# Optimization experiments

Hardware: AMD Instinct MI355X
Metric: run time of the kernel (lower is better)

Reference implementation:

```python
import jax, jax.numpy as jnp
import numpy as np

K = 4                      # options['num_k']
NOISE_EPS = 0.1            # noise_epsilon in noisy_top_k_gating
LOSS_COEF = 1e-4
EPS_COMBINE = float(np.finfo(np.float64).eps)  # np.finfo(float).eps in combine
INV_SQRT2 = 0.7071067811865475


def _norm_cdf(z):
    # Normal(0,1).cdf
    return 0.5 * (1.0 + jax.lax.erf(z * INV_SQRT2))


def _cv_squared(v):
    # torch .var() is unbiased (ddof=1)
    return jnp.var(v, ddof=1) / (jnp.mean(v) ** 2 + 1e-10)


def setup_inputs() -> dict:
    key = jax.random.key(0)
    B, D, E, H, O = 1024, 1024, 16, 2048, 1024
    ks = jax.random.split(key, 6)
    x = jax.random.normal(ks[0], (B, D), jnp.float32)
    w_gate = jax.random.normal(ks[1], (D, E), jnp.float32) * 0.02
    w_noise = jax.random.normal(ks[2], (D, E), jnp.float32) * 0.02
    W1 = jax.random.normal(ks[3], (E, D, H), jnp.float32) / np.sqrt(D).astype(np.float32)
    b1 = jnp.zeros((E, H), jnp.float32)
    W2 = jax.random.normal(ks[4], (E, H, O), jnp.float32) / np.sqrt(H).astype(np.float32)
    b2 = jnp.zeros((E, O), jnp.float32)
    noise = jax.random.normal(ks[5], (B, E), jnp.float32)  # randn_like(clean_logits)
    return {"x": x, "w_gate": w_gate, "w_noise": w_noise,
            "W1": W1, "b1": b1, "W2": W2, "b2": b2, "noise": noise}


def moe_forward(x, w_gate, w_noise, W1, b1, W2, b2, noise):
    B = x.shape[0]
    # --- noisy top-k gating (train=True path) ---
    clean_logits = x @ w_gate                              # [B, E]
    noise_std = jax.nn.softplus(x @ w_noise) + NOISE_EPS   # [B, E]
    noisy_logits = clean_logits + noise * noise_std        # [B, E]
    top_logits, top_idx = jax.lax.top_k(noisy_logits, K + 1)  # [B, K+1]
    topk_gates = jax.nn.softmax(top_logits[:, :K], axis=1)    # [B, K]
    gates = jnp.zeros_like(noisy_logits).at[
        jnp.arange(B)[:, None], top_idx[:, :K]].set(topk_gates)  # [B, E] sparse
    # --- load = E[prob in top-k] (smooth load estimate) ---
    thr_in = top_logits[:, K][:, None]       # (k+1)-th value: threshold if in
    thr_out = top_logits[:, K - 1][:, None]  # k-th value: threshold if out
    is_in = noisy_logits > thr_in
    prob_if_in = _norm_cdf((clean_logits - thr_in) / noise_std)
    prob_if_out = _norm_cdf((clean_logits - thr_out) / noise_std)
    load = jnp.where(is_in, prob_if_in, prob_if_out).sum(0)   # [E]
    importance = gates.sum(0)                                 # [E]
    loss = (_cv_squared(importance) + _cv_squared(load)) * LOSS_COEF
    # --- experts + combine ---
    # Dense all-expert compute; gates are exactly zero off the top-k so the
    # gate-weighted sum reproduces the sparse dispatch/index_add combine math.
    h = jax.nn.relu(jnp.einsum('bi,eih->beh', x, W1) + b1)    # [B, E, H]
    expert_out = jnp.einsum('beh,eho->beo', h, W2) + b2       # [B, E, O]
    # combine: sum_e gate[b,e] * exp(expert_out[b,e,:]); zeros -> eps; log
    combined = jnp.einsum('be,beo->bo', gates, jnp.exp(expert_out))  # [B, O]
    combined = jnp.where(combined == 0, EPS_COMBINE, combined)
    y = jnp.log(combined)
    return y, loss


def reference(x, w_gate, w_noise, W1, b1, W2, b2, noise):
    return moe_forward(x, w_gate, w_noise, W1, b1, W2, b2, noise)
```

## Files before the change

### kernel.cpp

```cpp
#include <hip/hip_runtime.h>
#include <cstdint>
#include <cstddef>

#define BTOK 1024
#define DDIM 1024
#define EEXP 16
#define HDIM 2048
#define ODIM 1024

typedef __bf16 bh;
typedef bh bh8 __attribute__((ext_vector_type(8)));
typedef bh bh4 __attribute__((ext_vector_type(4)));
typedef float fx4 __attribute__((ext_vector_type(4)));

__device__ __forceinline__ void gload16(const void* g, void* l) {
  __builtin_amdgcn_global_load_lds(
      (const __attribute__((address_space(1))) void*)g,
      (__attribute__((address_space(3))) void*)l, 16, 0, 0);
}

__global__ __launch_bounds__(256) void k_tcvt(const float* __restrict__ in,
                                              bh* __restrict__ out, int R, int C) {
  const int e = blockIdx.z;
  const int r0 = blockIdx.y * 64, c0 = blockIdx.x * 64;
  const float* pin = in + (size_t)e * R * C;
  bh* pout = out + (size_t)e * R * C;
  __shared__ __align__(16) bh t[64 * 65];
  const int tid = threadIdx.x;
#pragma unroll
  for (int rep = 0; rep < 4; ++rep) {
    int task = rep * 256 + tid;
    int r = task >> 4, c4 = task & 15;
    fx4 v = *(const fx4*)(pin + (size_t)(r0 + r) * C + c0 + c4 * 4);
    int base = r * 65 + c4 * 4;
#pragma unroll
    for (int u = 0; u < 4; ++u) t[base + u] = (bh)v[u];
  }
  __syncthreads();
#pragma unroll
  for (int rep = 0; rep < 4; ++rep) {
    int task = rep * 256 + tid;
    int cc = task >> 4, g2 = task & 15;
    bh4 o;
#pragma unroll
    for (int u = 0; u < 4; ++u) o[u] = t[(g2 * 4 + u) * 65 + cc];
    *(bh4*)(pout + (size_t)(c0 + cc) * R + r0 + g2 * 4) = o;
  }
}

__global__ __launch_bounds__(256) void k_gating(
    const float* __restrict__ x, const float* __restrict__ wg,
    const float* __restrict__ wn, const float* __restrict__ nz,
    bh* __restrict__ xbf, unsigned* __restrict__ cnt,
    int* __restrict__ tok_buck, float* __restrict__ gate_buck,
    float* __restrict__ imp_part, float* __restrict__ load_part) {
  const int b = blockIdx.x, tid = threadIdx.x;
  __shared__ __align__(16) float xs[1024];
  __shared__ float part[32][9];
  __shared__ float vals[32];
  fx4 v = *(const fx4*)(x + (size_t)b * 1024 + tid * 4);
  *(fx4*)(xs + tid * 4) = v;
  bh4 xb;
#pragma unroll
  for (int u = 0; u < 4; ++u) xb[u] = (bh)v[u];
  *(bh4*)(xbf + (size_t)b * 1024 + tid * 4) = xb;
  __syncthreads();
  const int col = tid & 31, g = tid >> 5;
  const float* wp = ((col < 16) ? wg : wn) + (col & 15);
  float s = 0.f;
  for (int it = g * 128; it < g * 128 + 128; ++it) s += xs[it] * wp[it * 16];
  part[col][g] = s;
  __syncthreads();
  if (tid < 32) {
    float tsum = 0.f;
#pragma unroll
    for (int gg = 0; gg < 8; ++gg) tsum += part[tid][gg];
    vals[tid] = tsum;
  }
  __syncthreads();
  if (tid == 0) {
    float clean[16], sd[16], noisy[16];
#pragma unroll
    for (int e = 0; e < 16; ++e) {
      clean[e] = vals[e];
      float raw = vals[16 + e];
      float sp = fmaxf(raw, 0.f) + log1pf(expf(-fabsf(raw)));
      sd[e] = sp + 0.1f;
      noisy[e] = clean[e] + nz[b * 16 + e] * sd[e];
    }
    float tv[5]; int ti[5]; unsigned used = 0;
    for (int r = 0; r < 5; ++r) {
      float bst = -INFINITY; int bi = 0;
      for (int e = 0; e < 16; ++e)
        if (!((used >> e) & 1u) && noisy[e] > bst) { bst = noisy[e]; bi = e; }
      used |= 1u << bi; tv[r] = bst; ti[r] = bi;
    }
    float gts[4]; float se = 0.f;
#pragma unroll
    for (int k = 0; k < 4; ++k) { gts[k] = expf(tv[k] - tv[0]); se += gts[k]; }
#pragma unroll
    for (int k = 0; k < 4; ++k) gts[k] /= se;
    const float thr_in = tv[4], thr_out = tv[3];
    float imp[16];
#pragma unroll
    for (int e = 0; e < 16; ++e) imp[e] = 0.f;
    for (int k = 0; k < 4; ++k) imp[ti[k]] = gts[k];
    for (int e = 0; e < 16; ++e) imp_part[b * 16 + e] = imp[e];
    for (int e = 0; e < 16; ++e) {
      bool is_in = noisy[e] > thr_in;
      float z = (clean[e] - (is_in ? thr_in : thr_out)) / sd[e];
      load_part[b * 16 + e] = 0.5f * (1.f + erff(z * 0.70710678118654752f));
    }
    for (int k = 0; k < 4; ++k) {
      int ee = ti[k];
      unsigned p = atomicAdd(&cnt[ee], 1u);
      tok_buck[ee * 1024 + (int)p] = b;
      gate_buck[ee * 1024 + (int)p] = gts[k];
    }
  }
}

__device__ __forceinline__ float cv2_16(const float* v) {
  float m = 0.f;
  for (int i = 0; i < 16; ++i) m += v[i];
  m *= (1.f / 16.f);
  float var = 0.f;
  for (int i = 0; i < 16; ++i) { float d = v[i] - m; var += d * d; }
  var *= (1.f / 15.f);
  return var / (m * m + 1e-10f);
}

__global__ __launch_bounds__(256) void k_finalize(
    const unsigned* __restrict__ cnt, unsigned* __restrict__ offs,
    const float* __restrict__ imp_part, const float* __restrict__ load_part,
    float* __restrict__ loss_out) {
  const int tid = threadIdx.x;
  __shared__ float red[256];
  __shared__ float impv[16], loadv[16];
  const int e = tid & 15, p = tid >> 4;
  float s = 0.f;
  for (int r = 0; r < 64; ++r) s += imp_part[((p * 64 + r) << 4) + e];
  red[tid] = s;
  __syncthreads();
  if (tid < 16) {
    float t = 0.f;
    for (int pp = 0; pp < 16; ++pp) t += red[pp * 16 + tid];
    impv[tid] = t;
  }
  __syncthreads();
  s = 0.f;
  for (int r = 0; r < 64; ++r) s += load_part[((p * 64 + r) << 4) + e];
  red[tid] = s;
  __syncthreads();
  if (tid < 16) {
    float t = 0.f;
    for (int pp = 0; pp < 16; ++pp) t += red[pp * 16 + tid];
    loadv[tid] = t;
  }
  __syncthreads();
  if (tid == 0) {
    unsigned o = 0;
    for (int ee = 0; ee < 16; ++ee) { offs[ee] = o; o += cnt[ee]; }
    loss_out[0] = (cv2_16(impv) + cv2_16(loadv)) * 1e-4f;
  }
}

__global__ __launch_bounds__(256) void k_gemm1(
    const bh* __restrict__ xbf, const bh* __restrict__ w1t,
    const float* __restrict__ b1, const int* __restrict__ tok_buck,
    const unsigned* __restrict__ cnt, const unsigned* __restrict__ offs,
    bh* __restrict__ hbf) {
  const int e = blockIdx.z, mt = blockIdx.y, nt = blockIdx.x;
  const int ne = (int)cnt[e];
  if (mt * 128 >= ne) return;
  __shared__ __align__(16) bh As[128 * 32];
  __shared__ __align__(16) bh Bs[128 * 32];
  const int tid = threadIdx.x;
  const int lane = tid & 63, wv = tid >> 6, wm = wv >> 1, wn_ = wv & 1;

  const bh* a_src[2]; const bh* b_src[2];
  void* a_dst[2]; void* b_dst[2];
#pragma unroll
  for (int r = 0; r < 2; ++r) {
    int task = r * 256 + tid;
    int row = task >> 2, s = task & 3;
    int gm = mt * 128 + row; if (gm >= ne) gm = ne - 1;
    int tok = tok_buck[e * 1024 + gm];
    a_src[r] = xbf + (size_t)tok * 1024 + ((s ^ (row & 3)) << 3);
    b_src[r] = w1t + (size_t)e * (2048 * 1024) + (size_t)(nt * 128 + row) * 1024 +
               ((s ^ (row & 3)) << 3);
    int wub = (r * 256 + (wv << 6)) << 4;
    a_dst[r] = (char*)As + wub;
    b_dst[r] = (char*)Bs + wub;
  }
  const int ln15 = lane & 15, q = lane >> 4;
  const int qs = ((q ^ (ln15 & 3)) << 3);
  int a_off[4], b_off[4];
#pragma unroll
  for (int i = 0; i < 4; ++i) {
    a_off[i] = (wm * 64 + i * 16 + ln15) * 32 + qs;
    b_off[i] = (wn_ * 64 + i * 16 + ln15) * 32 + qs;
  }
  fx4 zero = {0.f, 0.f, 0.f, 0.f};
  fx4 acc[4][4];
#pragma unroll
  for (int i = 0; i < 4; ++i)
#pragma unroll
    for (int j = 0; j < 4; ++j) acc[i][j] = zero;

  for (int kt = 0; kt < 32; ++kt) {
    __syncthreads();
    const int ko = kt * 32;
#pragma unroll
    for (int r = 0; r < 2; ++r) {
      gload16(a_src[r] + ko, a_dst[r]);
      gload16(b_src[r] + ko, b_dst[r]);
    }
    __syncthreads();
    bh8 af[4], bfr[4];
#pragma unroll
    for (int i = 0; i < 4; ++i) af[i] = *(const bh8*)(As + a_off[i]);
#pragma unroll
    for (int i = 0; i < 4; ++i) bfr[i] = *(const bh8*)(Bs + b_off[i]);
#pragma unroll
    for (int i = 0; i < 4; ++i)
#pragma unroll
      for (int j = 0; j < 4; ++j)
        acc[i][j] = __builtin_amdgcn_mfma_f32_16x16x32_bf16(af[i], bfr[j], acc[i][j], 0, 0, 0);
  }

  int nrows = ne - mt * 128; if (nrows > 128) nrows = 128;
  int jn[4]; float b1v[4];
#pragma unroll
  for (int j = 0; j < 4; ++j) {
    jn[j] = nt * 128 + wn_ * 64 + j * 16 + ln15;
    b1v[j] = b1[e * 2048 + jn[j]];
  }
  const int rowbase = (int)offs[e] + mt * 128;
#pragma unroll
  for (int i = 0; i < 4; ++i)
#pragma unroll
    for (int rr = 0; rr < 4; ++rr) {
      int ml = wm * 64 + i * 16 + q * 4 + rr;
      if (ml < nrows) {
        size_t ro = (size_t)(rowbase + ml) * 2048;
#pragma unroll
        for (int j = 0; j < 4; ++j) {
          float vv = acc[i][j][rr] + b1v[j];
          hbf[ro + jn[j]] = (bh)fmaxf(vv, 0.f);
        }
      }
    }
}

__global__ __launch_bounds__(256) void k_gemm2(
    const bh* __restrict__ hbf, const bh* __restrict__ w2t,
    const float* __restrict__ b2, const int* __restrict__ tok_buck,
    const float* __restrict__ gate_buck, const unsigned* __restrict__ cnt,
    const unsigned* __restrict__ offs, float* __restrict__ yv) {
  const int e = blockIdx.z, mt = blockIdx.y, nt = blockIdx.x;
  const int ne = (int)cnt[e];
  if (mt * 128 >= ne) return;
  __shared__ __align__(16) bh As[128 * 32];
  __shared__ __align__(16) bh Bs[128 * 32];
  const int tid = threadIdx.x;
  const int lane = tid & 63, wv = tid >> 6, wm = wv >> 1, wn_ = wv & 1;
  const int rowbase = (int)offs[e] + mt * 128;

  const bh* a_src[2]; const bh* b_src[2];
  void* a_dst[2]; void* b_dst[2];
#pragma unroll
  for (int r = 0; r < 2; ++r) {
    int task = r * 256 + tid;
    int row = task >> 2, s = task & 3;
    a_src[r] = hbf + (size_t)(rowbase + row) * 2048 + ((s ^ (row & 3)) << 3);
    b_src[r] = w2t + (size_t)e * (1024 * 2048) + (size_t)(nt * 128 + row) * 2048 +
               ((s ^ (row & 3)) << 3);
    int wub = (r * 256 + (wv << 6)) << 4;
    a_dst[r] = (char*)As + wub;
    b_dst[r] = (char*)Bs + wub;
  }
  const int ln15 = lane & 15, q = lane >> 4;
  const int qs = ((q ^ (ln15 & 3)) << 3);
  int a_off[4], b_off[4];
#pragma unroll
  for (int i = 0; i < 4; ++i) {
    a_off[i] = (wm * 64 + i * 16 + ln15) * 32 + qs;
    b_off[i] = (wn_ * 64 + i * 16 + ln15) * 32 + qs;
  }
  fx4 zero = {0.f, 0.f, 0.f, 0.f};
  fx4 acc[4][4];
#pragma unroll
  for (int i = 0; i < 4; ++i)
#pragma unroll
    for (int j = 0; j < 4; ++j) acc[i][j] = zero;

  for (int kt = 0; kt < 64; ++kt) {
    __syncthreads();
    const int ko = kt * 32;
#pragma unroll
    for (int r = 0; r < 2; ++r) {
      gload16(a_src[r] + ko, a_dst[r]);
      gload16(b_src[r] + ko, b_dst[r]);
    }
    __syncthreads();
    bh8 af[4], bfr[4];
#pragma unroll
    for (int i = 0; i < 4; ++i) af[i] = *(const bh8*)(As + a_off[i]);
#pragma unroll
    for (int i = 0; i < 4; ++i) bfr[i] = *(const bh8*)(Bs + b_off[i]);
#pragma unroll
    for (int i = 0; i < 4; ++i)
#pragma unroll
      for (int j = 0; j < 4; ++j)
        acc[i][j] = __builtin_amdgcn_mfma_f32_16x16x32_bf16(af[i], bfr[j], acc[i][j], 0, 0, 0);
  }

  int nrows = ne - mt * 128; if (nrows > 128) nrows = 128;
  int on[4]; float b2v[4];
#pragma unroll
  for (int j = 0; j < 4; ++j) {
    on[j] = nt * 128 + wn_ * 64 + j * 16 + ln15;
    b2v[j] = b2[e * 1024 + on[j]];
  }
#pragma unroll
  for (int i = 0; i < 4; ++i)
#pragma unroll
    for (int rr = 0; rr < 4; ++rr) {
      int ml = wm * 64 + i * 16 + q * 4 + rr;
      if (ml < nrows) {
        int pos = mt * 128 + ml;
        int bt = tok_buck[e * 1024 + pos];
        float gg = gate_buck[e * 1024 + pos];
        float* yrow = yv + (size_t)bt * 1024;
#pragma unroll
        for (int j = 0; j < 4; ++j)
          atomicAdd(&yrow[on[j]], gg * expf(acc[i][j][rr] + b2v[j]));
      }
    }
}

__global__ __launch_bounds__(256) void k_log(float* __restrict__ yv) {
  const int i = blockIdx.x * 256 + threadIdx.x;
  fx4* p = (fx4*)yv + i;
  fx4 v = *p;
#pragma unroll
  for (int c = 0; c < 4; ++c) {
    float w = v[c];
    if (w == 0.f) w = 2.2204460492503131e-16f;
    v[c] = logf(w);
  }
  *p = v;
}

extern "C" void kernel_launch(void* const* d_in, const int* in_sizes, int n_in,
                              void* d_out, int out_size, void* d_ws, size_t ws_size,
                              hipStream_t stream) {
  const float* x  = (const float*)d_in[0];
  const float* wg = (const float*)d_in[1];
  const float* wn = (const float*)d_in[2];
  const float* W1 = (const float*)d_in[3];
  const float* b1 = (const float*)d_in[4];
  const float* W2 = (const float*)d_in[5];
  const float* b2 = (const float*)d_in[6];
  const float* nz = (const float*)d_in[7];
  float* out = (float*)d_out;

  char* ws = (char*)d_ws;
  unsigned* cnt      = (unsigned*)(ws + 0);
  unsigned* offs     = (unsigned*)(ws + 64);
  float*    imp_part = (float*)(ws + 256);
  float*    load_part= (float*)(ws + 256 + 65536);
  int*      tok_buck = (int*)(ws + 256 + 2 * 65536);
  float*    gate_buck= (float*)(ws + 256 + 3 * 65536);
  bh*       xbf      = (bh*)(ws + 262400);
  bh*       hbf      = (bh*)(ws + 2359552);
  bh*       w1t      = (bh*)(ws + 19661056);
  bh*       w2t      = (bh*)(ws + 86769920);
  const size_t needed = 153878784;
  if (ws_size < needed) {
    hipMemsetAsync(d_out, 0x42, (size_t)out_size * 4, stream);
    return;
  }

  hipMemsetAsync(d_out, 0, (size_t)out_size * 4, stream);
  hipMemsetAsync(cnt, 0, 64, stream);

  k_tcvt<<<dim3(2048 / 64, 1024 / 64, 16), 256, 0, stream>>>(W1, w1t, 1024, 2048);
  k_tcvt<<<dim3(1024 / 64, 2048 / 64, 16), 256, 0, stream>>>(W2, w2t, 2048, 1024);
  k_gating<<<1024, 256, 0, stream>>>(x, wg, wn, nz, xbf, cnt, tok_buck, gate_buck,
                                     imp_part, load_part);
  k_finalize<<<1, 256, 0, stream>>>(cnt, offs, imp_part, load_part, out + (out_size - 1));
  k_gemm1<<<dim3(16, 8, 16), 256, 0, stream>>>(xbf, w1t, b1, tok_buck, cnt, offs, hbf);
  k_gemm2<<<dim3(8, 8, 16), 256, 0, stream>>>(hbf, w2t, b2, tok_buck, gate_buck, cnt, offs, out);
  k_log<<<1024, 256, 0, stream>>>(out);
}
```

Measured before the change: 491.5 us.

## Replace LDS-staged expert GEMMs with register-prefetched direct global loads

Both expert GEMM kernels drop the shared-memory tile staging and its two barriers per k-step. Each wave now loads its MFMA fragments straight from global memory into registers through a 4-deep software prefetch ring. The N tile shrinks from 128 to 64 to double the grid, and launch bounds request 2 blocks per SM. The cost is that the 4 waves no longer share A and B tiles through LDS, so global and L2 traffic per FLOP goes up, and the prefetch buffers raise register pressure.

```diff
diff --git a/kernel.cpp b/kernel.cpp
--- a/kernel.cpp
+++ b/kernel.cpp
@@ -1,23 +1,11 @@
 #include <hip/hip_runtime.h>
 #include <cstdint>
 #include <cstddef>
-
-#define BTOK 1024
-#define DDIM 1024
-#define EEXP 16
-#define HDIM 2048
-#define ODIM 1024
 
 typedef __bf16 bh;
 typedef bh bh8 __attribute__((ext_vector_type(8)));
 typedef bh bh4 __attribute__((ext_vector_type(4)));
 typedef float fx4 __attribute__((ext_vector_type(4)));
-
-__device__ __forceinline__ void gload16(const void* g, void* l) {
-  __builtin_amdgcn_global_load_lds(
-      (const __attribute__((address_space(1))) void*)g,
-      (__attribute__((address_space(3))) void*)l, 16, 0, 0);
-}
 
 __global__ __launch_bounds__(256) void k_tcvt(const float* __restrict__ in,
                                               bh* __restrict__ out, int R, int C) {
@@ -165,7 +153,9 @@
   }
 }
 
-__global__ __launch_bounds__(256) void k_gemm1(
+#define PF 4
+
+__global__ __launch_bounds__(256, 2) void k_gemm1r(
     const bh* __restrict__ xbf, const bh* __restrict__ w1t,
     const float* __restrict__ b1, const int* __restrict__ tok_buck,
     const unsigned* __restrict__ cnt, const unsigned* __restrict__ offs,
@@ -173,75 +163,73 @@
   const int e = blockIdx.z, mt = blockIdx.y, nt = blockIdx.x;
   const int ne = (int)cnt[e];
   if (mt * 128 >= ne) return;
-  __shared__ __align__(16) bh As[128 * 32];
-  __shared__ __align__(16) bh Bs[128 * 32];
   const int tid = threadIdx.x;
-  const int lane = tid & 63, wv = tid >> 6, wm = wv >> 1, wn_ = wv & 1;
-
-  const bh* a_src[2]; const bh* b_src[2];
-  void* a_dst[2]; void* b_dst[2];
-#pragma unroll
-  for (int r = 0; r < 2; ++r) {
-    int task = r * 256 + tid;
-    int row = task >> 2, s = task & 3;
-    int gm = mt * 128 + row; if (gm >= ne) gm = ne - 1;
+  const int lane = tid & 63, wv = tid >> 6;
+  const int ln15 = lane & 15, q = lane >> 4;
+  const int NK = 32;
+
+  const bh* ap[2];
+#pragma unroll
+  for (int i = 0; i < 2; ++i) {
+    int gm = mt * 128 + wv * 32 + i * 16 + ln15;
+    if (gm >= ne) gm = ne - 1;
     int tok = tok_buck[e * 1024 + gm];
-    a_src[r] = xbf + (size_t)tok * 1024 + ((s ^ (row & 3)) << 3);
-    b_src[r] = w1t + (size_t)e * (2048 * 1024) + (size_t)(nt * 128 + row) * 1024 +
-               ((s ^ (row & 3)) << 3);
-    int wub = (r * 256 + (wv << 6)) << 4;
-    a_dst[r] = (char*)As + wub;
-    b_dst[r] = (char*)Bs + wub;
-  }
-  const int ln15 = lane & 15, q = lane >> 4;
-  const int qs = ((q ^ (ln15 & 3)) << 3);
-  int a_off[4], b_off[4];
-#pragma unroll
-  for (int i = 0; i < 4; ++i) {
-    a_off[i] = (wm * 64 + i * 16 + ln15) * 32 + qs;
-    b_off[i] = (wn_ * 64 + i * 16 + ln15) * 32 + qs;
-  }
+    ap[i] = xbf + (size_t)tok * 1024 + q * 8;
+  }
+  const bh* bp[4];
+#pragma unroll
+  for (int j = 0; j < 4; ++j) {
+    int n = nt * 64 + j * 16 + ln15;
+    bp[j] = w1t + (size_t)e * (2048 * 1024) + (size_t)n * 1024 + q * 8;
+  }
+
   fx4 zero = {0.f, 0.f, 0.f, 0.f};
-  fx4 acc[4][4];
-#pragma unroll
-  for (int i = 0; i < 4; ++i)
+  fx4 acc[2][4];
+#pragma unroll
+  for (int i = 0; i < 2; ++i)
 #pragma unroll
     for (int j = 0; j < 4; ++j) acc[i][j] = zero;
 
-  for (int kt = 0; kt < 32; ++kt) {
-    __syncthreads();
-    const int ko = kt * 32;
-#pragma unroll
-    for (int r = 0; r < 2; ++r) {
-      gload16(a_src[r] + ko, a_dst[r]);
-      gload16(b_src[r] + ko, b_dst[r]);
-    }
-    __syncthreads();
-    bh8 af[4], bfr[4];
-#pragma unroll
-    for (int i = 0; i < 4; ++i) af[i] = *(const bh8*)(As + a_off[i]);
-#pragma unroll
-    for (int i = 0; i < 4; ++i) bfr[i] = *(const bh8*)(Bs + b_off[i]);
-#pragma unroll
-    for (int i = 0; i < 4; ++i)
-#pragma unroll
-      for (int j = 0; j < 4; ++j)
-        acc[i][j] = __builtin_amdgcn_mfma_f32_16x16x32_bf16(af[i], bfr[j], acc[i][j], 0, 0, 0);
+  bh8 stA[PF][2], stB[PF][4];
+#pragma unroll
+  for (int s = 0; s < PF; ++s) {
+#pragma unroll
+    for (int i = 0; i < 2; ++i) stA[s][i] = *(const bh8*)(ap[i] + s * 32);
+#pragma unroll
+    for (int j = 0; j < 4; ++j) stB[s][j] = *(const bh8*)(bp[j] + s * 32);
+  }
+  for (int kt0 = 0; kt0 < NK; kt0 += PF) {
+#pragma unroll
+    for (int u = 0; u < PF; ++u) {
+      const int kt = kt0 + u;
+#pragma unroll
+      for (int i = 0; i < 2; ++i)
+#pragma unroll
+        for (int j = 0; j < 4; ++j)
+          acc[i][j] = __builtin_amdgcn_mfma_f32_16x16x32_bf16(stA[u][i], stB[u][j], acc[i][j], 0, 0, 0);
+      const int kn = kt + PF;
+      if (kn < NK) {
+#pragma unroll
+        for (int i = 0; i < 2; ++i) stA[u][i] = *(const bh8*)(ap[i] + kn * 32);
+#pragma unroll
+        for (int j = 0; j < 4; ++j) stB[u][j] = *(const bh8*)(bp[j] + kn * 32);
+      }
+    }
   }
 
   int nrows = ne - mt * 128; if (nrows > 128) nrows = 128;
   int jn[4]; float b1v[4];
 #pragma unroll
   for (int j = 0; j < 4; ++j) {
-    jn[j] = nt * 128 + wn_ * 64 + j * 16 + ln15;
+    jn[j] = nt * 64 + j * 16 + ln15;
     b1v[j] = b1[e * 2048 + jn[j]];
   }
   const int rowbase = (int)offs[e] + mt * 128;
 #pragma unroll
-  for (int i = 0; i < 4; ++i)
+  for (int i = 0; i < 2; ++i)
 #pragma unroll
     for (int rr = 0; rr < 4; ++rr) {
-      int ml = wm * 64 + i * 16 + q * 4 + rr;
+      int ml = wv * 32 + i * 16 + q * 4 + rr;
       if (ml < nrows) {
         size_t ro = (size_t)(rowbase + ml) * 2048;
 #pragma unroll
@@ -253,7 +241,7 @@
     }
 }
 
-__global__ __launch_bounds__(256) void k_gemm2(
+__global__ __launch_bounds__(256, 2) void k_gemm2r(
     const bh* __restrict__ hbf, const bh* __restrict__ w2t,
     const float* __restrict__ b2, const int* __restrict__ tok_buck,
     const float* __restrict__ gate_buck, const unsigned* __restrict__ cnt,
@@ -261,73 +249,72 @@
   const int e = blockIdx.z, mt = blockIdx.y, nt = blockIdx.x;
   const int ne = (int)cnt[e];
   if (mt * 128 >= ne) return;
-  __shared__ __align__(16) bh As[128 * 32];
-  __shared__ __align__(16) bh Bs[128 * 32];
   const int tid = threadIdx.x;
-  const int lane = tid & 63, wv = tid >> 6, wm = wv >> 1, wn_ = wv & 1;
+  const int lane = tid & 63, wv = tid >> 6;
+  const int ln15 = lane & 15, q = lane >> 4;
+  const int NK = 64;
+  int nrows = ne - mt * 128; if (nrows > 128) nrows = 128;
   const int rowbase = (int)offs[e] + mt * 128;
 
-  const bh* a_src[2]; const bh* b_src[2];
-  void* a_dst[2]; void* b_dst[2];
-#pragma unroll
-  for (int r = 0; r < 2; ++r) {
-    int task = r * 256 + tid;
-    int row = task >> 2, s = task & 3;
-    a_src[r] = hbf + (size_t)(rowbase + row) * 2048 + ((s ^ (row & 3)) << 3);
-    b_src[r] = w2t + (size_t)e * (1024 * 2048) + (size_t)(nt * 128 + row) * 2048 +
-               ((s ^ (row & 3)) << 3);
-    int wub = (r * 256 + (wv << 6)) << 4;
-    a_dst[r] = (char*)As + wub;
-    b_dst[r] = (char*)Bs + wub;
-  }
-  const int ln15 = lane & 15, q = lane >> 4;
-  const int qs = ((q ^ (ln15 & 3)) << 3);
-  int a_off[4], b_off[4];
-#pragma unroll
-  for (int i = 0; i < 4; ++i) {
-    a_off[i] = (wm * 64 + i * 16 + ln15) * 32 + qs;
-    b_off[i] = (wn_ * 64 + i * 16 + ln15) * 32 + qs;
-  }
+  const bh* ap[2];
+#pragma unroll
+  for (int i = 0; i < 2; ++i) {
+    int ml = wv * 32 + i * 16 + ln15;
+    if (ml >= nrows) ml = nrows - 1;
+    ap[i] = hbf + (size_t)(rowbase + ml) * 2048 + q * 8;
+  }
+  const bh* bp[4];
+#pragma unroll
+  for (int j = 0; j < 4; ++j) {
+    int n = nt * 64 + j * 16 + ln15;
+    bp[j] = w2t + (size_t)e * (1024 * 2048) + (size_t)n * 2048 + q * 8;
+  }
+
   fx4 zero = {0.f, 0.f, 0.f, 0.f};
-  fx4 acc[4][4];
-#pragma unroll
-  for (int i = 0; i < 4; ++i)
+  fx4 acc[2][4];
+#pragma unroll
+  for (int i = 0; i < 2; ++i)
 #pragma unroll
     for (int j = 0; j < 4; ++j) acc[i][j] = zero;
 
-  for (int kt = 0; kt < 64; ++kt) {
-    __syncthreads();
-    const int ko = kt * 32;
-#pragma unroll
-    for (int r = 0; r < 2; ++r) {
-      gload16(a_src[r] + ko, a_dst[r]);
-      gload16(b_src[r] + ko, b_dst[r]);
-    }
-    __syncthreads();
-    bh8 af[4], bfr[4];
-#pragma unroll
-    for (int i = 0; i < 4; ++i) af[i] = *(const bh8*)(As + a_off[i]);
-#pragma unroll
-    for (int i = 0; i < 4; ++i) bfr[i] = *(const bh8*)(Bs + b_off[i]);
-#pragma unroll
-    for (int i = 0; i < 4; ++i)
-#pragma unroll
-      for (int j = 0; j < 4; ++j)
-        acc[i][j] = __builtin_amdgcn_mfma_f32_16x16x32_bf16(af[i], bfr[j], acc[i][j], 0, 0, 0);
-  }
-
-  int nrows = ne - mt * 128; if (nrows > 128) nrows = 128;
+  bh8 stA[PF][2], stB[PF][4];
+#pragma unroll
+  for (int s = 0; s < PF; ++s) {
+#pragma unroll
+    for (int i = 0; i < 2; ++i) stA[s][i] = *(const bh8*)(ap[i] + s * 32);
+#pragma unroll
+    for (int j = 0; j < 4; ++j) stB[s][j] = *(const bh8*)(bp[j] + s * 32);
+  }
+  for (int kt0 = 0; kt0 < NK; kt0 += PF) {
+#pragma unroll
+    for (int u = 0; u < PF; ++u) {
+      const int kt = kt0 + u;
+#pragma unroll
+      for (int i = 0; i < 2; ++i)
+#pragma unroll
+        for (int j = 0; j < 4; ++j)
+          acc[i][j] = __builtin_amdgcn_mfma_f32_16x16x32_bf16(stA[u][i], stB[u][j], acc[i][j], 0, 0, 0);
+      const int kn = kt + PF;
+      if (kn < NK) {
+#pragma unroll
+        for (int i = 0; i < 2; ++i) stA[u][i] = *(const bh8*)(ap[i] + kn * 32);
+#pragma unroll
+        for (int j = 0; j < 4; ++j) stB[u][j] = *(const bh8*)(bp[j] + kn * 32);
+      }
+    }
+  }
+
   int on[4]; float b2v[4];
 #pragma unroll
   for (int j = 0; j < 4; ++j) {
-    on[j] = nt * 128 + wn_ * 64 + j * 16 + ln15;
+    on[j] = nt * 64 + j * 16 + ln15;
     b2v[j] = b2[e * 1024 + on[j]];
   }
 #pragma unroll
-  for (int i = 0; i < 4; ++i)
+  for (int i = 0; i < 2; ++i)
 #pragma unroll
     for (int rr = 0; rr < 4; ++rr) {
-      int ml = wm * 64 + i * 16 + q * 4 + rr;
+      int ml = wv * 32 + i * 16 + q * 4 + rr;
       if (ml < nrows) {
         int pos = mt * 128 + ml;
         int bt = tok_buck[e * 1024 + pos];
@@ -391,7 +378,7 @@
   k_gating<<<1024, 256, 0, stream>>>(x, wg, wn, nz, xbf, cnt, tok_buck, gate_buck,
                                      imp_part, load_part);
   k_finalize<<<1, 256, 0, stream>>>(cnt, offs, imp_part, load_part, out + (out_size - 1));
-  k_gemm1<<<dim3(16, 8, 16), 256, 0, stream>>>(xbf, w1t, b1, tok_buck, cnt, offs, hbf);
-  k_gemm2<<<dim3(8, 8, 16), 256, 0, stream>>>(hbf, w2t, b2, tok_buck, gate_buck, cnt, offs, out);
+  k_gemm1r<<<dim3(32, 8, 16), 256, 0, stream>>>(xbf, w1t, b1, tok_buck, cnt, offs, hbf);
+  k_gemm2r<<<dim3(16, 8, 16), 256, 0, stream>>>(hbf, w2t, b2, tok_buck, gate_buck, cnt, offs, out);
   k_log<<<1024, 256, 0, stream>>>(out);
 }
```

Result: slower. 706.7 us (+43.8%).
